# Optimization experiments

Measured on AMD Instinct MI355X. Metric: run time of the kernel, lower is better.

The kernel has to match this reference:

```python
import jax, jax.numpy as jnp
import numpy as np

EPS = 1e-5
COMMIT_W = 2.0
LATENT = 64


def _conv1d(x, w, b, stride, padding):
    # x: [B,C,T], w: [O,I,K] (torch Conv1d layout)
    y = jax.lax.conv_general_dilated(x, w, (stride,), [(padding, padding)],
                                     dimension_numbers=('NCH', 'OIH', 'NCH'))
    return y + b[None, :, None]


def _bn(x, g, b):
    # training-mode BatchNorm1d: batch statistics over (B, T) per channel
    mu = x.mean(axis=(0, 2), keepdims=True)
    var = x.var(axis=(0, 2), keepdims=True)
    return (x - mu) * jax.lax.rsqrt(var + EPS) * g[None, :, None] + b[None, :, None]


def setup_inputs():
    key = jax.random.key(0)
    ks = jax.random.split(key, 10)
    B, T, D, K = 8, 10240, LATENT, 8192
    f32 = jnp.float32
    def n(k, shape, scale):
        return jax.random.normal(k, shape, dtype=f32) * scale
    return {
        'x': jax.random.normal(ks[0], (B, 1, T), dtype=f32),
        'enc_w1': n(ks[1], (16, 1, 5), 0.3), 'enc_b1': jnp.zeros((16,), f32),
        'bn1_g': jnp.ones((16,), f32), 'bn1_b': jnp.zeros((16,), f32),
        'enc_w2': n(ks[2], (32, 16, 5), 0.1), 'enc_b2': jnp.zeros((32,), f32),
        'bn2_g': jnp.ones((32,), f32), 'bn2_b': jnp.zeros((32,), f32),
        'enc_w3': n(ks[3], (64, 32, 25), 0.05), 'enc_b3': jnp.zeros((64,), f32),
        'bn3_g': jnp.ones((64,), f32), 'bn3_b': jnp.zeros((64,), f32),
        'codebook': jax.random.normal(ks[4], (K, D), dtype=f32),
        'dec_wt': n(ks[5], (64, 64, 25), 0.05),  # torch ConvTranspose1d [in,out,k]
        'dbn1_g': jnp.ones((64,), f32), 'dbn1_b': jnp.zeros((64,), f32),
        'dec_w2': n(ks[6], (64, 64, 5), 0.08), 'dec_b2': jnp.zeros((64,), f32),
        'dbn2_g': jnp.ones((64,), f32), 'dbn2_b': jnp.zeros((64,), f32),
        'dec_w3': n(ks[7], (1, 64, 1), 0.1), 'dec_b3': jnp.zeros((1,), f32),
    }


def reference(x, enc_w1, enc_b1, bn1_g, bn1_b, enc_w2, enc_b2, bn2_g, bn2_b,
              enc_w3, enc_b3, bn3_g, bn3_b, codebook, dec_wt, dbn1_g, dbn1_b,
              dec_w2, dec_b2, dbn2_g, dbn2_b, dec_w3, dec_b3):
    # ---- encoder ----
    h = jax.nn.silu(_conv1d(x, enc_w1, enc_b1, 1, 2))
    h = _bn(h, bn1_g, bn1_b)
    h = jax.nn.silu(_conv1d(h, enc_w2, enc_b2, 1, 2))
    h = _bn(h, bn2_g, bn2_b)
    h = jnp.tanh(_conv1d(h, enc_w3, enc_b3, 5, 12))
    z = _bn(h, bn3_g, bn3_b)                       # [B, 64, L]
    B, _, L = z.shape
    # ---- VQ: euclidean nearest-neighbor against codebook ----
    zf = z.transpose(0, 2, 1).reshape(-1, LATENT)  # [N, D]
    d = ((zf * zf).sum(-1, keepdims=True)
         - 2.0 * zf @ codebook.T
         + (codebook * codebook).sum(-1)[None, :])  # [N, K]
    idx = jnp.argmin(d, axis=-1)                   # [N]
    q = codebook[idx]                              # [N, D]
    commit_loss = COMMIT_W * jnp.mean((jax.lax.stop_gradient(q) - zf) ** 2)
    q_st = zf + jax.lax.stop_gradient(q - zf)      # straight-through
    zq = q_st.reshape(B, L, LATENT).transpose(0, 2, 1)  # [B, 64, L]
    # ---- decoder ----
    # ConvTranspose1d(k=25, s=5, p=12) == dilated conv with flipped kernel
    wconv = jnp.flip(dec_wt, -1).transpose(1, 0, 2)     # [out, in, k]
    h = jax.lax.conv_general_dilated(zq, wconv, (1,), [(12, 12)], lhs_dilation=(5,),
                                     dimension_numbers=('NCH', 'OIH', 'NCH'))
    h = jax.nn.silu(h)
    h = _bn(h, dbn1_g, dbn1_b)
    h = jax.nn.silu(_conv1d(h, dec_w2, dec_b2, 1, 2))
    h = _bn(h, dbn2_g, dbn2_b)
    recon = _conv1d(h, dec_w3, dec_b3, 1, 0)       # [B, 1, ~T]
    T = x.shape[2]
    cur = recon.shape[2]
    if cur > T:
        recon = recon[:, :, :T]
    elif cur < T:
        recon = jnp.pad(recon, ((0, 0), (0, 0), (0, T - cur)))
    return recon, idx.reshape(B, L), commit_loss
```

## Files before the change

### kernel.cpp

```cpp
#include <hip/hip_runtime.h>
#include <hip/hip_bf16.h>

#define DEV __device__ __forceinline__

typedef __attribute__((ext_vector_type(8))) short s8v;
typedef __attribute__((ext_vector_type(16))) float f32x16;
typedef __attribute__((address_space(1))) const unsigned int u32g;
typedef __attribute__((address_space(3))) unsigned int u32l;

DEV void gl_lds(const void* g, void* l){
  __builtin_amdgcn_global_load_lds((u32g*)g, (u32l*)l, 16, 0, 0);
}

DEV float siluf(float x){ return x / (1.f + expf(-x)); }

DEV float wredsum(float v){
  #pragma unroll
  for(int m = 32; m; m >>= 1) v += __shfl_xor(v, m);
  return v;
}

DEV unsigned short bf16rne(float f){
  unsigned int u = __float_as_uint(f);
  u += 0x7FFFu + ((u >> 16) & 1u);
  return (unsigned short)(u >> 16);
}
DEV float bf16tof(unsigned short h){ return __uint_as_float(((unsigned int)h) << 16); }

DEV unsigned umed3(unsigned a, unsigned b, unsigned c){
  unsigned d;
  asm("v_med3_u32 %0, %1, %2, %3" : "=v"(d) : "v"(a), "v"(b), "v"(c));
  return d;
}

#define S1 0
#define Q1 16
#define S2 32
#define Q2 64
#define S3 96
#define Q3 160
#define S4 224
#define Q4 288
#define S5 352
#define Q5 416
#define SLOSS 480
#define NSTATF 512

#define EPSQ 6u
#define NCHUNK 8

__global__ void k_prep(const float* ew3, const float* dwt, float* w3t, float* dwtt,
                       unsigned short* wb7){
  const int n1 = 64*32*25, n2 = 64*64*25;
  for(int i = blockIdx.x*blockDim.x + threadIdx.x; i < n1+n2; i += gridDim.x*blockDim.x){
    if(i < n1){
      int c = i/(32*25), r = i - c*(32*25), ii = r/25, k = r - ii*25;
      w3t[(ii*25 + k)*64 + c] = ew3[i];
    } else {
      int j = i - n1;
      int ii = j/(64*25), r = j - ii*(64*25), o = r/25, k = r - o*25;
      float w = dwt[j];
      dwtt[(ii*25 + k)*64 + o] = w;
      wb7[((size_t)(k*64 + o))*64 + ii] = bf16rne(w);
    }
  }
}

__global__ void k_prep2(const float* __restrict__ cb, unsigned short* __restrict__ cbsw,
                        float* __restrict__ cnw, float* __restrict__ cnw2,
                        unsigned short* __restrict__ cbb, int* cnt){
  if(blockIdx.x == 0 && threadIdx.x == 0) *cnt = 0;
  int j = blockIdx.x*256 + threadIdx.x;
  if(j < 8192){
    float nrm = 0.f;
    unsigned swz = (j & 15) << 4;
    char* rowp = (char*)cbsw + (size_t)j*256;
    #pragma unroll
    for(int k = 0; k < 64; k++){
      float x = cb[(size_t)j*64 + k];
      unsigned short hi = bf16rne(x);
      float lo = x - bf16tof(hi);
      *(unsigned short*)(rowp + (((unsigned)(2*k)) ^ swz)) = hi;
      *(unsigned short*)(rowp + (((unsigned)(128 + 2*k)) ^ swz)) = bf16rne(lo);
      cbb[(size_t)j*64 + k] = hi;
      nrm = fmaf(x, x, nrm);
    }
    cnw[j] = nrm;
    cnw2[j] = (nrm + 1024.f) * 256.f;
  }
}

__global__ void k1(const float* __restrict__ x, const float* __restrict__ w1,
                   const float* __restrict__ b1, float* __restrict__ h1, float* stats){
  __shared__ float xs[136];
  __shared__ float ssum[16], ssq[16];
  int tid = threadIdx.x, b = blockIdx.y, t0 = blockIdx.x*128;
  if(tid < 16){ ssum[tid] = 0.f; ssq[tid] = 0.f; }
  for(int i = tid; i < 132; i += 256){
    int t = t0 + i - 2;
    xs[i] = (t >= 0 && t < 10240) ? x[b*10240 + t] : 0.f;
  }
  __syncthreads();
  int c = tid & 15, sgrp = tid >> 4;
  float w[5];
  #pragma unroll
  for(int k = 0; k < 5; k++) w[k] = w1[c*5 + k];
  float bias = b1[c];
  float outv[8];
  float ps = 0.f, pq = 0.f;
  #pragma unroll
  for(int s = 0; s < 8; s++){
    float a = bias;
    #pragma unroll
    for(int k = 0; k < 5; k++) a = fmaf(w[k], xs[sgrp*8 + s + k], a);
    a = siluf(a);
    outv[s] = a;
    ps += a; pq += a*a;
  }
  float* op = h1 + ((size_t)(b*16 + c))*10240 + t0 + sgrp*8;
  #pragma unroll
  for(int q = 0; q < 2; q++)
    *(float4*)(op + q*4) = make_float4(outv[q*4], outv[q*4+1], outv[q*4+2], outv[q*4+3]);
  ps += __shfl_xor(ps, 16); pq += __shfl_xor(pq, 16);
  ps += __shfl_xor(ps, 32); pq += __shfl_xor(pq, 32);
  if((tid & 48) == 0){ atomicAdd(&ssum[c], ps); atomicAdd(&ssq[c], pq); }
  __syncthreads();
  if(tid < 16){ atomicAdd(stats+S1+tid, ssum[tid]); atomicAdd(stats+Q1+tid, ssq[tid]); }
}

__global__ __launch_bounds__(256) void k2(const float* __restrict__ h1,
                   const float* __restrict__ w2, const float* __restrict__ b2,
                   const float* __restrict__ g1, const float* __restrict__ bb1,
                   float* __restrict__ h2out, float* stats){
  __shared__ float hs[16][136];
  __shared__ float A1s[16], B1s[16];
  __shared__ float ssum[32], ssq[32];
  int tid = threadIdx.x, b = blockIdx.y, t0 = blockIdx.x*128;
  if(tid < 16){
    float mu = stats[S1+tid]/81920.f;
    float var = stats[Q1+tid]/81920.f - mu*mu;
    float rs = rsqrtf(var + 1e-5f);
    A1s[tid] = rs*g1[tid];
    B1s[tid] = bb1[tid] - mu*rs*g1[tid];
  }
  if(tid < 32){ ssum[tid] = 0.f; ssq[tid] = 0.f; }
  __syncthreads();
  {
    int ch = tid >> 4, j0 = tid & 15;
    float A = A1s[ch], B = B1s[ch];
    const float* hp = h1 + ((size_t)(b*16 + ch))*10240;
    for(int j = j0; j < 132; j += 16){
      int t = t0 + j - 2;
      hs[ch][j] = (t >= 0 && t < 10240) ? hp[t]*A + B : 0.f;
    }
  }
  __syncthreads();
  int c = tid & 31, tgrp = tid >> 5;
  int tb = tgrp*16;
  float acc[16];
  float bias = b2[c];
  #pragma unroll
  for(int s = 0; s < 16; s++) acc[s] = bias;
  for(int ic = 0; ic < 4; ic++){
    float wf[20];
    const float* wp = w2 + c*80 + ic*20;
    #pragma unroll
    for(int q = 0; q < 5; q++) *(float4*)(wf + q*4) = *(const float4*)(wp + q*4);
    #pragma unroll
    for(int di = 0; di < 4; di++){
      int i = ic*4 + di;
      float z[20];
      #pragma unroll
      for(int q = 0; q < 5; q++) *(float4*)(z + q*4) = *(const float4*)(&hs[i][tb] + q*4);
      float w0 = wf[di*5], w1 = wf[di*5+1], w2v = wf[di*5+2], w3 = wf[di*5+3], w4 = wf[di*5+4];
      #pragma unroll
      for(int s = 0; s < 16; s++)
        acc[s] = fmaf(w0, z[s], fmaf(w1, z[s+1], fmaf(w2v, z[s+2],
                 fmaf(w3, z[s+3], fmaf(w4, z[s+4], acc[s])))));
    }
  }
  float ps = 0.f, pq = 0.f;
  #pragma unroll
  for(int s = 0; s < 16; s++){
    float a = siluf(acc[s]);
    acc[s] = a;
    ps += a; pq += a*a;
  }
  float* op = h2out + ((size_t)(b*32 + c))*10240 + t0 + tb;
  #pragma unroll
  for(int q = 0; q < 4; q++)
    *(float4*)(op + q*4) = make_float4(acc[q*4], acc[q*4+1], acc[q*4+2], acc[q*4+3]);
  ps += __shfl_xor(ps, 32); pq += __shfl_xor(pq, 32);
  if((tid & 32) == 0){ atomicAdd(&ssum[c], ps); atomicAdd(&ssq[c], pq); }
  __syncthreads();
  if(tid < 32){ atomicAdd(stats+S2+tid, ssum[tid]); atomicAdd(stats+Q2+tid, ssq[tid]); }
}

__global__ void k3(const float* __restrict__ h2, const float* __restrict__ w3t,
                   const float* __restrict__ eb3, const float* __restrict__ g2,
                   const float* __restrict__ bb2, float* __restrict__ zn, float* stats){
  __shared__ __align__(16) float X[5*32*24];
  __shared__ float A2[32], B2[32];
  __shared__ float ssum[64], ssq[64];
  int tid = threadIdx.x, b = blockIdx.y, l0 = blockIdx.x*16;
  if(tid < 32){
    float mu = stats[S2+tid]/81920.f;
    float var = stats[Q2+tid]/81920.f - mu*mu;
    float rs = rsqrtf(var + 1e-5f);
    A2[tid] = rs*g2[tid];
    B2[tid] = bb2[tid] - mu*rs*g2[tid];
  }
  if(tid < 64){ ssum[tid] = 0.f; ssq[tid] = 0.f; }
  __syncthreads();
  for(int i2 = tid; i2 < 5*32*20; i2 += 256){
    int kk = i2/640;
    int r  = i2 - kk*640;
    int ch = r/20, m = r - ch*20;
    int t = 5*(l0 + m) + kk - 12;
    float v = 0.f;
    if(t >= 0 && t < 10240) v = h2[((b*32+ch)*10240)+t]*A2[ch] + B2[ch];
    X[(kk*32+ch)*24 + m] = v;
  }
  __syncthreads();
  int c = tid & 63, lslot = tid >> 6;
  float acc[4];
  float bias = eb3[c];
  #pragma unroll
  for(int s = 0; s < 4; s++) acc[s] = bias;
  for(int i = 0; i < 32; i++){
    #pragma unroll
    for(int kk = 0; kk < 5; kk++){
      const float* xp = &X[(kk*32+i)*24 + lslot*4];
      float4 za = *(const float4*)(xp);
      float4 zb = *(const float4*)(xp + 4);
      float z[8] = {za.x,za.y,za.z,za.w,zb.x,zb.y,zb.z,zb.w};
      #pragma unroll
      for(int kap = 0; kap < 5; kap++){
        float w = w3t[(i*25 + kap*5 + kk)*64 + c];
        #pragma unroll
        for(int s = 0; s < 4; s++) acc[s] = fmaf(w, z[s+kap], acc[s]);
      }
    }
  }
  float ls = 0.f, lq = 0.f;
  #pragma unroll
  for(int s = 0; s < 4; s++){
    int l = l0 + lslot*4 + s;
    float a = tanhf(acc[s]);
    zn[((b*2048 + l)*64) + c] = a;
    ls += a; lq += a*a;
  }
  atomicAdd(&ssum[c], ls); atomicAdd(&ssq[c], lq);
  __syncthreads();
  if(tid < 64){ atomicAdd(stats+S3+tid, ssum[tid]); atomicAdd(stats+Q3+tid, ssq[tid]); }
}

__global__ __launch_bounds__(256, 3) void k5m(const float* __restrict__ zn,
    const unsigned short* __restrict__ cbsw, const float* __restrict__ cnw2,
    const float* __restrict__ g3, const float* __restrict__ b3,
    const float* __restrict__ stats,
    unsigned int* __restrict__ pbk, unsigned int* __restrict__ psk){
  __shared__ __align__(16) unsigned char cbuf[2][16384];
  __shared__ float A3s[64], B3s[64];
  int tid = threadIdx.x;
  int chunk = blockIdx.x;
  int m0 = blockIdx.y * 128;
  int lane = tid & 63, wr = tid >> 6;
  int h = lane >> 5, cll = lane & 31;
  int row = m0 + wr*32 + cll;

  if(tid < 64){
    float mu = stats[S3+tid]/16384.f;
    float var = stats[Q3+tid]/16384.f - mu*mu;
    float rs = rsqrtf(var + 1e-5f);
    A3s[tid] = rs*g3[tid];
    B3s[tid] = b3[tid] - mu*rs*g3[tid];
  }

  int c0 = chunk * 1024;
  const char* csrc = (const char*)cbsw + (size_t)c0*256;
  #pragma unroll
  for(int c2 = 0; c2 < 4; c2++)
    gl_lds(csrc + c2*4096 + tid*16, &cbuf[0][0] + c2*4096 + tid*16);
  __syncthreads();

  s8v ah[4], al[4];
  const float* zp = zn + (size_t)row*64;
  #pragma unroll
  for(int s = 0; s < 4; s++){
    int koff = s*16 + h*8;
    float4 v0 = *(const float4*)(zp + koff);
    float4 v1 = *(const float4*)(zp + koff + 4);
    float vv[8] = {v0.x,v0.y,v0.z,v0.w,v1.x,v1.y,v1.z,v1.w};
    #pragma unroll
    for(int i = 0; i < 8; i++){
      float v = fmaf(vv[i], A3s[koff + i], B3s[koff + i]);
      unsigned short hi = bf16rne(v);
      ah[s][i] = (short)hi;
      al[s][i] = (short)bf16rne(v - bf16tof(hi));
    }
  }

  unsigned int bk[16], sk[16];
  #pragma unroll
  for(int r = 0; r < 16; r++){ bk[r] = 0xFFFFFFFFu; sk[r] = 0xFFFFFFFFu; }
  f32x16 zv;
  #pragma unroll
  for(int i = 0; i < 16; i++) zv[i] = 0.f;

  unsigned swz = (unsigned)(cll & 15) << 4;
  for(int tile = 0; tile < 16; ++tile){
    int bsel = tile & 1;
    if(tile < 15){
      const char* ns = csrc + (size_t)(tile+1)*16384;
      #pragma unroll
      for(int c2 = 0; c2 < 4; c2++)
        gl_lds(ns + c2*4096 + tid*16, &cbuf[bsel^1][0] + c2*4096 + tid*16);
    }
    #pragma unroll
    for(int half = 0; half < 2; half++){
      const unsigned char* bp = &cbuf[bsel][0] + (half*32 + cll)*256;
      s8v bh[4], bl[4];
      #pragma unroll
      for(int s = 0; s < 4; s++){
        bh[s] = *(const s8v*)(bp + (((unsigned)(s*32 + h*16)) ^ swz));
        bl[s] = *(const s8v*)(bp + (((unsigned)(128 + s*32 + h*16)) ^ swz));
      }
      unsigned col = (unsigned)(c0 + tile*64 + half*32 + cll);
      float cnv2 = cnw2[col];
      f32x16 a1 = __builtin_amdgcn_mfma_f32_32x32x16_bf16(ah[0], bh[0], zv, 0, 0, 0);
      f32x16 a2 = __builtin_amdgcn_mfma_f32_32x32x16_bf16(al[0], bh[0], zv, 0, 0, 0);
      a2 = __builtin_amdgcn_mfma_f32_32x32x16_bf16(ah[0], bl[0], a2, 0, 0, 0);
      #pragma unroll
      for(int s = 1; s < 4; s++){
        a1 = __builtin_amdgcn_mfma_f32_32x32x16_bf16(ah[s], bh[s], a1, 0, 0, 0);
        a2 = __builtin_amdgcn_mfma_f32_32x32x16_bf16(al[s], bh[s], a2, 0, 0, 0);
        a2 = __builtin_amdgcn_mfma_f32_32x32x16_bf16(ah[s], bl[s], a2, 0, 0, 0);
      }
      #pragma unroll
      for(int r = 0; r < 16; r++){
        float q = fmaf(-512.f, a1[r], cnv2);
        q = fmaf(-512.f, a2[r], q);
        q = fminf(q, 524287.f);
        unsigned k = (((unsigned)q) << 13) | col;
        unsigned nb = bk[r] < k ? bk[r] : k;
        sk[r] = umed3(sk[r], bk[r], k);
        bk[r] = nb;
      }
    }
    __syncthreads();
  }

  #pragma unroll
  for(int m = 1; m <= 16; m <<= 1){
    #pragma unroll
    for(int r = 0; r < 16; r++){
      unsigned int ob = (unsigned int)__shfl_xor((int)bk[r], m);
      unsigned int os = (unsigned int)__shfl_xor((int)sk[r], m);
      unsigned int s2 = sk[r] < os ? sk[r] : os;
      sk[r] = umed3(s2, bk[r], ob);
      bk[r] = bk[r] < ob ? bk[r] : ob;
    }
  }
  if(cll == 0){
    size_t base = (size_t)chunk*16384 + m0 + wr*32 + 4*h;
    #pragma unroll
    for(int r = 0; r < 16; r++){
      int lr = (r&3) + 8*(r>>2);
      pbk[base + lr] = bk[r];
      psk[base + lr] = sk[r];
    }
  }
}

__global__ void k5r(const unsigned int* __restrict__ pbk,
                    const unsigned int* __restrict__ psk, int* __restrict__ idxw,
                    float* __restrict__ out_idx, int* __restrict__ list, int* cnt){
  int row = blockIdx.x*256 + threadIdx.x;
  unsigned int bk = pbk[row], sk = psk[row];
  #pragma unroll
  for(int c = 1; c < NCHUNK; c++){
    unsigned int ob = pbk[(size_t)c*16384 + row];
    unsigned int os = psk[(size_t)c*16384 + row];
    unsigned int s2 = sk < os ? sk : os;
    sk = umed3(s2, bk, ob);
    bk = bk < ob ? bk : ob;
  }
  int idx = (int)(bk & 0x1FFFu);
  idxw[row] = idx;
  out_idx[row] = (float)idx;
  if((sk >> 13) - (bk >> 13) <= EPSQ){
    int p = atomicAdd(cnt, 1);
    list[p] = row;
  }
}

__global__ __launch_bounds__(256) void k5x(const float* __restrict__ zn,
    const float* __restrict__ cb, const float* __restrict__ cnw,
    const float* __restrict__ g3, const float* __restrict__ b3,
    const float* __restrict__ stats,
    const int* __restrict__ list, const int* cnt,
    float* __restrict__ pxd, int* __restrict__ pxi){
  __shared__ float A3s[64], B3s[64];
  int tid = threadIdx.x;
  if(tid < 64){
    float mu = stats[S3+tid]/16384.f;
    float var = stats[Q3+tid]/16384.f - mu*mu;
    float rs = rsqrtf(var + 1e-5f);
    A3s[tid] = rs*g3[tid];
    B3s[tid] = b3[tid] - mu*rs*g3[tid];
  }
  __syncthreads();
  int chunk = blockIdx.x;
  int n = *cnt;
  int rgrp = tid >> 6, cs = tid & 63;
  int c0 = chunk * 1024;
  for(int bat = blockIdx.y; bat*4 < n; bat += 256){
    int e = bat*4 + rgrp;
    int ec = e < n ? e : n-1;
    int row = list[ec];
    float4 zr[16];
    const float4* zp = (const float4*)(zn + (size_t)row*64);
    #pragma unroll
    for(int q = 0; q < 16; q++){
      float4 v = zp[q];
      v.x = fmaf(v.x, A3s[q*4+0], B3s[q*4+0]);
      v.y = fmaf(v.y, A3s[q*4+1], B3s[q*4+1]);
      v.z = fmaf(v.z, A3s[q*4+2], B3s[q*4+2]);
      v.w = fmaf(v.w, A3s[q*4+3], B3s[q*4+3]);
      zr[q] = v;
    }
    float bd = 3.4e38f; int bi = 0;
    for(int step = 0; step < 16; step++){
      int j = c0 + step*64 + cs;
      const float4* cp = (const float4*)(cb + (size_t)j*64);
      float cnv = cnw[j];
      float da = 0.f, db = 0.f;
      #pragma unroll
      for(int q = 0; q < 16; q += 2){
        float4 ca = cp[q], cb4 = cp[q+1];
        da = fmaf(ca.x, zr[q].x, da);  da = fmaf(ca.y, zr[q].y, da);
        da = fmaf(ca.z, zr[q].z, da);  da = fmaf(ca.w, zr[q].w, da);
        db = fmaf(cb4.x, zr[q+1].x, db); db = fmaf(cb4.y, zr[q+1].y, db);
        db = fmaf(cb4.z, zr[q+1].z, db); db = fmaf(cb4.w, zr[q+1].w, db);
      }
      float d = fmaf(-2.f, da + db, cnv);
      if(d < bd){ bd = d; bi = j; }
    }
    #pragma unroll
    for(int m = 1; m <= 32; m <<= 1){
      float od = __shfl_xor(bd, m);
      int   oi = __shfl_xor(bi, m);
      if(od < bd || (od == bd && oi < bi)){ bd = od; bi = oi; }
    }
    if(cs == 0 && e < n){
      pxd[(size_t)chunk*16384 + e] = bd;
      pxi[(size_t)chunk*16384 + e] = bi;
    }
  }
}

__global__ void k5x2(const float* __restrict__ pxd, const int* __restrict__ pxi,
                     const int* __restrict__ list, const int* cnt,
                     int* __restrict__ idxw, float* __restrict__ out_idx){
  int e = blockIdx.x*256 + threadIdx.x;
  int n = *cnt;
  if(e >= n) return;
  float bd = pxd[e]; int bi = pxi[e];
  #pragma unroll
  for(int c = 1; c < NCHUNK; c++){
    float od = pxd[(size_t)c*16384 + e];
    int   oi = pxi[(size_t)c*16384 + e];
    if(od < bd || (od == bd && oi < bi)){ bd = od; bi = oi; }
  }
  int row = list[e];
  idxw[row] = bi;
  out_idx[row] = (float)bi;
}

__global__ void k_loss(const float* __restrict__ zn, const float* __restrict__ cb,
                       const float* __restrict__ g3, const float* __restrict__ b3,
                       const int* __restrict__ idxw, float* stats){
  __shared__ float A3s[64], B3s[64];
  int tid = threadIdx.x;
  if(tid < 64){
    float mu = stats[S3+tid]/16384.f;
    float var = stats[Q3+tid]/16384.f - mu*mu;
    float rs = rsqrtf(var + 1e-5f);
    A3s[tid] = rs*g3[tid];
    B3s[tid] = b3[tid] - mu*rs*g3[tid];
  }
  __syncthreads();
  int row = blockIdx.x*256 + tid;
  int code = idxw[row];
  const float* cp = cb + (size_t)code*64;
  const float* zp = zn + (size_t)row*64;
  float s = 0.f;
  #pragma unroll
  for(int k = 0; k < 64; k++){
    float v = fmaf(zp[k], A3s[k], B3s[k]);
    float dd = cp[k] - v;
    s = fmaf(dd, dd, s);
  }
  float tot = wredsum(s);
  if((tid & 63) == 0) atomicAdd(stats + SLOSS, tot);
}

__global__ __launch_bounds__(320) void k7m(const int* __restrict__ idxp,
    const unsigned short* __restrict__ cbb, const unsigned short* __restrict__ wb7,
    unsigned short* __restrict__ h4t, float* stats){
  __shared__ __align__(16) unsigned char lA[37*128];
  __shared__ float tb[5*64*33];
  __shared__ float ssum[64], ssq[64];
  int tid = threadIdx.x, b = blockIdx.y, u0 = blockIdx.x*32;
  if(tid < 64){ ssum[tid] = 0.f; ssq[tid] = 0.f; }
  {
    int m = tid >> 3, part = tid & 7;
    if(m < 37){
      int u = u0 - 2 + m;
      uint4 val = make_uint4(0,0,0,0);
      if(u >= 0 && u < 2048){
        int code = idxp[b*2048 + u];
        val = *(const uint4*)((const char*)cbb + (size_t)code*128 + part*16);
      }
      *(uint4*)(lA + m*128 + (((unsigned)(part*16)) ^ (((unsigned)m & 7) << 4))) = val;
    }
  }
  __syncthreads();
  int lane = tid & 63, h = lane >> 5, cl = lane & 31;
  int v = tid >> 6;
  const int km[5]  = {2,3,4,0,1};
  const int ovv[5] = {2,2,2,3,3};
  f32x16 acc0, acc1;
  #pragma unroll
  for(int i = 0; i < 16; i++){ acc0[i] = 0.f; acc1[i] = 0.f; }
  #pragma unroll
  for(int r = 0; r < 5; r++){
    int off = ovv[v] - r + 2;
    int m = cl + off;
    unsigned aswz = ((unsigned)m & 7) << 4;
    int k = km[v] + 5*r;
    const char* b0p = (const char*)wb7 + (size_t)(k*64 + cl)*128;
    const char* b1p = b0p + 32*128;
    #pragma unroll
    for(int s = 0; s < 4; s++){
      unsigned o = (unsigned)(s*32 + h*16);
      s8v a  = *(const s8v*)(lA + m*128 + (o ^ aswz));
      s8v b0 = *(const s8v*)(b0p + o);
      s8v b1 = *(const s8v*)(b1p + o);
      acc0 = __builtin_amdgcn_mfma_f32_32x32x16_bf16(a, b0, acc0, 0, 0, 0);
      acc1 = __builtin_amdgcn_mfma_f32_32x32x16_bf16(a, b1, acc1, 0, 0, 0);
    }
  }
  float ps0 = 0.f, pq0 = 0.f, ps1 = 0.f, pq1 = 0.f;
  #pragma unroll
  for(int r = 0; r < 16; r++){
    int ul = (r&3) + 8*(r>>2) + 4*h;
    int u = u0 + ul;
    float v0 = siluf(acc0[r]), v1 = siluf(acc1[r]);
    tb[(v*64 + cl)*33 + ul]      = v0;
    tb[(v*64 + 32 + cl)*33 + ul] = v1;
    if(v == 0 || u < 2047){ ps0 += v0; pq0 += v0*v0; ps1 += v1; pq1 += v1*v1; }
  }
  atomicAdd(&ssum[cl], ps0);      atomicAdd(&ssq[cl], pq0);
  atomicAdd(&ssum[32 + cl], ps1); atomicAdd(&ssq[32 + cl], pq1);
  __syncthreads();
  if(tid < 64){ atomicAdd(stats+S4+tid, ssum[tid]); atomicAdd(stats+Q4+tid, ssq[tid]); }
  #pragma unroll
  for(int j = 0; j < 16; j++){
    int flat = j*320 + tid;
    int tl = flat >> 5;
    int chp = flat & 31;
    int t = u0*5 + tl;
    if(t < 10236){
      int vv = tl % 5, ul = tl / 5;
      float f0 = tb[(vv*64 + 2*chp)*33 + ul];
      float f1 = tb[(vv*64 + 2*chp + 1)*33 + ul];
      unsigned int pk = (unsigned int)bf16rne(f0) | ((unsigned int)bf16rne(f1) << 16);
      size_t rowb = ((size_t)b*10248 + 2 + t)*128;
      *(unsigned int*)((char*)h4t + rowb + (((unsigned)(4*chp)) ^ (((unsigned)t & 7) << 4))) = pk;
    }
  }
}

__global__ void k8w(const float* __restrict__ w2d, const float* __restrict__ b2d,
                    const float* __restrict__ g4, const float* __restrict__ bb4,
                    const float* __restrict__ stats, unsigned short* __restrict__ wbt,
                    float* __restrict__ beta, unsigned int* __restrict__ h4tz){
  __shared__ float A4[64], B4[64];
  int tid = threadIdx.x;
  for(int i = tid; i < 3072; i += 256){
    int b = i / 384, r = i - b*384;
    int row12 = r >> 5, word = r & 31;
    int row = row12 < 2 ? row12 : 10236 + row12;
    h4tz[((size_t)b*10248 + row)*32 + word] = 0u;
  }
  if(tid < 64){
    float mu = stats[S4+tid]/81888.f;
    float var = stats[Q4+tid]/81888.f - mu*mu;
    float rs = rsqrtf(var + 1e-5f);
    A4[tid] = rs*g4[tid];
    B4[tid] = bb4[tid] - mu*rs*g4[tid];
  }
  __syncthreads();
  for(int e = tid; e < 64*64*5; e += 256){
    int c = e/320, r = e - c*320, i = r/5, k = r - i*5;
    unsigned short hw = bf16rne(w2d[e] * A4[i]);
    int row = k*64 + c;
    *(unsigned short*)((char*)wbt + (size_t)row*128 + (((unsigned)(2*i)) ^ (((unsigned)c & 7) << 4))) = hw;
  }
  if(tid < 64){
    float s = b2d[tid];
    for(int i = 0; i < 64; i++){
      float wsum = 0.f;
      #pragma unroll
      for(int k = 0; k < 5; k++) wsum += w2d[(tid*64 + i)*5 + k];
      s += wsum * B4[i];
    }
    beta[tid] = s;
  }
}

__global__ __launch_bounds__(256) void k8(const unsigned short* __restrict__ h4t,
    const unsigned short* __restrict__ wbt, const float* __restrict__ beta,
    unsigned short* __restrict__ h5b, float* stats){
  __shared__ __align__(16) unsigned char lA[68*128];
  __shared__ float ssum[64], ssq[64];
  int tid = threadIdx.x, b = blockIdx.y, t0 = blockIdx.x*64;
  if(tid < 64){ ssum[tid] = 0.f; ssq[tid] = 0.f; }
  const char* srcA = (const char*)h4t + ((size_t)b*10248 + t0)*128;
  #pragma unroll
  for(int c2 = 0; c2 < 2; c2++)
    gl_lds(srcA + c2*4096 + tid*16, lA + c2*4096 + tid*16);
  if(tid < 32) gl_lds(srcA + 8192 + tid*16, lA + 8192 + tid*16);
  __syncthreads();

  int lane = tid & 63, h = lane >> 5, cl = lane & 31;
  int widx = tid >> 6;
  int wt0 = (widx >> 1) * 32;
  int wch = (widx & 1) * 32;
  f32x16 acc;
  #pragma unroll
  for(int i = 0; i < 16; i++) acc[i] = 0.f;
  unsigned bswz = (unsigned)(cl & 7) << 4;
  #pragma unroll
  for(int k = 0; k < 5; k++){
    int l = wt0 + cl + k;
    unsigned aswz = (unsigned)((l + 6) & 7) << 4;
    const char* bp = (const char*)wbt + (size_t)(k*64 + wch + cl)*128;
    #pragma unroll
    for(int s = 0; s < 4; s++){
      unsigned o = (unsigned)(s*32 + h*16);
      s8v a  = *(const s8v*)(lA + l*128 + (o ^ aswz));
      s8v bb = *(const s8v*)(bp + (o ^ bswz));
      acc = __builtin_amdgcn_mfma_f32_32x32x16_bf16(a, bb, acc, 0, 0, 0);
    }
  }
  float bet = beta[wch + cl];
  float ps = 0.f, pq = 0.f;
  #pragma unroll
  for(int r = 0; r < 16; r++){
    int t = t0 + wt0 + (r&3) + 8*(r>>2) + 4*h;
    float v0 = siluf(acc[r] + bet);
    if(t < 10236){
      h5b[((size_t)b*10240 + t)*64 + wch + cl] = bf16rne(v0);
      ps += v0; pq += v0*v0;
    }
  }
  atomicAdd(&ssum[wch + cl], ps); atomicAdd(&ssq[wch + cl], pq);
  __syncthreads();
  if(tid < 64){ atomicAdd(stats+S5+tid, ssum[tid]); atomicAdd(stats+Q5+tid, ssq[tid]); }
}

__global__ void k9(const unsigned short* __restrict__ h5b, const float* __restrict__ w3,
                   const float* __restrict__ b3, const float* __restrict__ g5,
                   const float* __restrict__ bb5, const float* stats,
                   float* __restrict__ out){
  __shared__ float WA[64], WB[64];
  int tid = threadIdx.x;
  if(blockIdx.x == 0 && blockIdx.y == 0 && tid == 0)
    out[98304] = 2.f * stats[SLOSS] / 1048576.f;
  if(tid < 64){
    float mu = stats[S5+tid]/81888.f;
    float var = stats[Q5+tid]/81888.f - mu*mu;
    float rs = rsqrtf(var + 1e-5f);
    float A = rs*g5[tid], B = bb5[tid] - mu*rs*g5[tid];
    float w = w3[tid];
    WA[tid] = w*A; WB[tid] = w*B;
  }
  __syncthreads();
  int b = blockIdx.y;
  int t = blockIdx.x*256 + tid;
  float acc = b3[0];
  if(t < 10236){
    const unsigned short* hp = h5b + ((size_t)b*10240 + t)*64;
    #pragma unroll
    for(int q = 0; q < 8; q++){
      uint4 u = *(const uint4*)(hp + q*8);
      unsigned int ua[4] = {u.x, u.y, u.z, u.w};
      #pragma unroll
      for(int w = 0; w < 4; w++){
        int c = q*8 + w*2;
        acc += WA[c]*bf16tof((unsigned short)(ua[w] & 0xFFFFu)) + WB[c];
        acc += WA[c+1]*bf16tof((unsigned short)(ua[w] >> 16)) + WB[c+1];
      }
    }
  } else acc = 0.f;
  out[b*10240 + t] = acc;
}

extern "C" void kernel_launch(void* const* d_in, const int* in_sizes, int n_in,
                              void* d_out, int out_size, void* d_ws, size_t ws_size,
                              hipStream_t stream){
  const float* x   = (const float*)d_in[0];
  const float* ew1 = (const float*)d_in[1];
  const float* eb1 = (const float*)d_in[2];
  const float* g1  = (const float*)d_in[3];
  const float* bb1 = (const float*)d_in[4];
  const float* ew2 = (const float*)d_in[5];
  const float* eb2 = (const float*)d_in[6];
  const float* g2  = (const float*)d_in[7];
  const float* bb2 = (const float*)d_in[8];
  const float* ew3 = (const float*)d_in[9];
  const float* eb3 = (const float*)d_in[10];
  const float* g3  = (const float*)d_in[11];
  const float* bb3 = (const float*)d_in[12];
  const float* cb  = (const float*)d_in[13];
  const float* dwt = (const float*)d_in[14];
  const float* g4  = (const float*)d_in[15];
  const float* bb4 = (const float*)d_in[16];
  const float* w2d = (const float*)d_in[17];
  const float* b2d = (const float*)d_in[18];
  const float* g5  = (const float*)d_in[19];
  const float* bb5 = (const float*)d_in[20];
  const float* w3d = (const float*)d_in[21];
  const float* b3d = (const float*)d_in[22];

  char* ws = (char*)d_ws;
  float* h1   = (float*)(ws + 0);
  unsigned short* cbsw = (unsigned short*)(ws + 0);
  float* cnw  = (float*)(ws + 2097152);
  float* cnw2 = (float*)(ws + 2129920);
  float* h2   = (float*)(ws + 5242880);
  float* zn   = (float*)(ws + 15728640);
  unsigned short* h4t = (unsigned short*)(ws + 0);
  unsigned short* h5b = (unsigned short*)(ws + 20971520);
  int*   list = (int*)  (ws + 20971520);
  int*   cnt  = (int*)  (ws + 21037056);
  unsigned int* pbk = (unsigned int*)(ws + 21037312);
  unsigned int* psk = (unsigned int*)(ws + 21561600);
  float* pxd  = (float*)(ws + 22085888);
  int*   pxi  = (int*)  (ws + 22610176);
  unsigned short* wbt = (unsigned short*)(ws + 31457280);
  float* beta = (float*)(ws + 31498240);
  unsigned short* wb7 = (unsigned short*)(ws + 32000000);
  unsigned short* cbb = (unsigned short*)(ws + 32300032);
  float* w3t  = (float*)(ws + 41934848);
  float* dwtt = (float*)(ws + 42139648);
  int*   idxw = (int*)  (ws + 42549248);
  float* stats= (float*)(ws + 42614784);
  if(ws_size < 42616832) return;

  float* out = (float*)d_out;

  hipMemsetAsync(stats, 0, NSTATF*4, stream);
  k_prep<<<600, 256, 0, stream>>>(ew3, dwt, w3t, dwtt, wb7);
  k1<<<dim3(80,8), 256, 0, stream>>>(x, ew1, eb1, h1, stats);
  k2<<<dim3(80,8), 256, 0, stream>>>(h1, ew2, eb2, g1, bb1, h2, stats);
  k_prep2<<<32, 256, 0, stream>>>(cb, cbsw, cnw, cnw2, cbb, cnt);
  k3<<<dim3(128,8), 256, 0, stream>>>(h2, w3t, eb3, g2, bb2, zn, stats);
  k5m<<<dim3(NCHUNK,128), 256, 0, stream>>>(zn, cbsw, cnw2, g3, bb3, stats, pbk, psk);
  k5r<<<64, 256, 0, stream>>>(pbk, psk, idxw, out + 81920, list, cnt);
  k5x<<<dim3(NCHUNK,256), 256, 0, stream>>>(zn, cb, cnw, g3, bb3, stats, list, cnt, pxd, pxi);
  k5x2<<<64, 256, 0, stream>>>(pxd, pxi, list, cnt, idxw, out + 81920);
  k_loss<<<64, 256, 0, stream>>>(zn, cb, g3, bb3, idxw, stats);
  k7m<<<dim3(64,8), 320, 0, stream>>>(idxw, cbb, wb7, h4t, stats);
  k8w<<<1, 256, 0, stream>>>(w2d, b2d, g4, bb4, stats, wbt, beta, (unsigned int*)h4t);
  k8<<<dim3(160,8), 256, 0, stream>>>(h4t, wbt, beta, h5b, stats);
  k9<<<dim3(40,8), 256, 0, stream>>>(h5b, w3d, b3d, g5, bb5, stats, out);
}
```

Measured before the change: 330.3 us.

## Widen k3 output tile, vectorize weight loads, merge k5m MFMA accumulators

The k3 encoder conv now computes 8 outputs per thread over 32-position blocks and reads its five tap weights per (channel, phase) as one packed vector from a re-laid-out weight array. This gives more reuse of each weight and LDS value and fewer scalar global loads, at the cost of more registers and a grid of half the size. In k5m the two accumulator chains are merged into one, freeing 16 VGPRs, and launch bounds are raised to 4 blocks per CU for occupancy. The merged chain is a longer serial MFMA dependency, and the hi/lo partial sums are now added in a different order. The unused dwtt transpose is also dropped.

Result: slower. 337.4 us (+2.2%).

```diff
diff --git a/kernel.cpp b/kernel.cpp
--- a/kernel.cpp
+++ b/kernel.cpp
@@ -49,19 +49,18 @@
 #define EPSQ 6u
 #define NCHUNK 8
 
-__global__ void k_prep(const float* ew3, const float* dwt, float* w3t, float* dwtt,
+__global__ void k_prep(const float* ew3, const float* dwt, float* w3t8,
                        unsigned short* wb7){
   const int n1 = 64*32*25, n2 = 64*64*25;
   for(int i = blockIdx.x*blockDim.x + threadIdx.x; i < n1+n2; i += gridDim.x*blockDim.x){
     if(i < n1){
       int c = i/(32*25), r = i - c*(32*25), ii = r/25, k = r - ii*25;
-      w3t[(ii*25 + k)*64 + c] = ew3[i];
+      int kk = k % 5, kap = k / 5;
+      w3t8[(((size_t)(ii*5 + kk))*64 + c)*8 + kap] = ew3[i];
     } else {
       int j = i - n1;
       int ii = j/(64*25), r = j - ii*(64*25), o = r/25, k = r - o*25;
-      float w = dwt[j];
-      dwtt[(ii*25 + k)*64 + o] = w;
-      wb7[((size_t)(k*64 + o))*64 + ii] = bf16rne(w);
+      wb7[((size_t)(k*64 + o))*64 + ii] = bf16rne(dwt[j]);
     }
   }
 }
@@ -196,13 +195,13 @@
   if(tid < 32){ atomicAdd(stats+S2+tid, ssum[tid]); atomicAdd(stats+Q2+tid, ssq[tid]); }
 }
 
-__global__ void k3(const float* __restrict__ h2, const float* __restrict__ w3t,
+__global__ void k3(const float* __restrict__ h2, const float* __restrict__ w3t8,
                    const float* __restrict__ eb3, const float* __restrict__ g2,
                    const float* __restrict__ bb2, float* __restrict__ zn, float* stats){
-  __shared__ __align__(16) float X[5*32*24];
+  __shared__ __align__(16) float X[5*32*40];
   __shared__ float A2[32], B2[32];
   __shared__ float ssum[64], ssq[64];
-  int tid = threadIdx.x, b = blockIdx.y, l0 = blockIdx.x*16;
+  int tid = threadIdx.x, b = blockIdx.y, l0 = blockIdx.x*32;
   if(tid < 32){
     float mu = stats[S2+tid]/81920.f;
     float var = stats[Q2+tid]/81920.f - mu*mu;
@@ -212,40 +211,44 @@
   }
   if(tid < 64){ ssum[tid] = 0.f; ssq[tid] = 0.f; }
   __syncthreads();
-  for(int i2 = tid; i2 < 5*32*20; i2 += 256){
-    int kk = i2/640;
-    int r  = i2 - kk*640;
-    int ch = r/20, m = r - ch*20;
+  for(int i2 = tid; i2 < 5*32*36; i2 += 256){
+    int kk = i2/1152;
+    int r  = i2 - kk*1152;
+    int ch = r/36, m = r - ch*36;
     int t = 5*(l0 + m) + kk - 12;
     float v = 0.f;
     if(t >= 0 && t < 10240) v = h2[((b*32+ch)*10240)+t]*A2[ch] + B2[ch];
-    X[(kk*32+ch)*24 + m] = v;
+    X[(kk*32+ch)*40 + m] = v;
   }
   __syncthreads();
   int c = tid & 63, lslot = tid >> 6;
-  float acc[4];
+  float acc[8];
   float bias = eb3[c];
   #pragma unroll
-  for(int s = 0; s < 4; s++) acc[s] = bias;
+  for(int s = 0; s < 8; s++) acc[s] = bias;
   for(int i = 0; i < 32; i++){
     #pragma unroll
     for(int kk = 0; kk < 5; kk++){
-      const float* xp = &X[(kk*32+i)*24 + lslot*4];
-      float4 za = *(const float4*)(xp);
-      float4 zb = *(const float4*)(xp + 4);
-      float z[8] = {za.x,za.y,za.z,za.w,zb.x,zb.y,zb.z,zb.w};
+      const float* xp = &X[(kk*32+i)*40 + lslot*8];
+      float z[12];
+      #pragma unroll
+      for(int q = 0; q < 3; q++) *(float4*)(z + q*4) = *(const float4*)(xp + q*4);
+      const float* wp = w3t8 + (((size_t)(i*5 + kk))*64 + c)*8;
+      float wv[5];
+      *(float4*)wv = *(const float4*)wp;
+      wv[4] = wp[4];
       #pragma unroll
       for(int kap = 0; kap < 5; kap++){
-        float w = w3t[(i*25 + kap*5 + kk)*64 + c];
+        float w = wv[kap];
         #pragma unroll
-        for(int s = 0; s < 4; s++) acc[s] = fmaf(w, z[s+kap], acc[s]);
+        for(int s = 0; s < 8; s++) acc[s] = fmaf(w, z[s+kap], acc[s]);
       }
     }
   }
   float ls = 0.f, lq = 0.f;
   #pragma unroll
-  for(int s = 0; s < 4; s++){
-    int l = l0 + lslot*4 + s;
+  for(int s = 0; s < 8; s++){
+    int l = l0 + lslot*8 + s;
     float a = tanhf(acc[s]);
     zn[((b*2048 + l)*64) + c] = a;
     ls += a; lq += a*a;
@@ -255,7 +258,7 @@
   if(tid < 64){ atomicAdd(stats+S3+tid, ssum[tid]); atomicAdd(stats+Q3+tid, ssq[tid]); }
 }
 
-__global__ __launch_bounds__(256, 3) void k5m(const float* __restrict__ zn,
+__global__ __launch_bounds__(256, 4) void k5m(const float* __restrict__ zn,
     const unsigned short* __restrict__ cbsw, const float* __restrict__ cnw2,
     const float* __restrict__ g3, const float* __restrict__ b3,
     const float* __restrict__ stats,
@@ -328,19 +331,18 @@
       }
       unsigned col = (unsigned)(c0 + tile*64 + half*32 + cll);
       float cnv2 = cnw2[col];
-      f32x16 a1 = __builtin_amdgcn_mfma_f32_32x32x16_bf16(ah[0], bh[0], zv, 0, 0, 0);
-      f32x16 a2 = __builtin_amdgcn_mfma_f32_32x32x16_bf16(al[0], bh[0], zv, 0, 0, 0);
-      a2 = __builtin_amdgcn_mfma_f32_32x32x16_bf16(ah[0], bl[0], a2, 0, 0, 0);
+      f32x16 a = __builtin_amdgcn_mfma_f32_32x32x16_bf16(ah[0], bl[0], zv, 0, 0, 0);
+      a = __builtin_amdgcn_mfma_f32_32x32x16_bf16(al[0], bh[0], a, 0, 0, 0);
+      a = __builtin_amdgcn_mfma_f32_32x32x16_bf16(ah[0], bh[0], a, 0, 0, 0);
       #pragma unroll
       for(int s = 1; s < 4; s++){
-        a1 = __builtin_amdgcn_mfma_f32_32x32x16_bf16(ah[s], bh[s], a1, 0, 0, 0);
-        a2 = __builtin_amdgcn_mfma_f32_32x32x16_bf16(al[s], bh[s], a2, 0, 0, 0);
-        a2 = __builtin_amdgcn_mfma_f32_32x32x16_bf16(ah[s], bl[s], a2, 0, 0, 0);
+        a = __builtin_amdgcn_mfma_f32_32x32x16_bf16(ah[s], bl[s], a, 0, 0, 0);
+        a = __builtin_amdgcn_mfma_f32_32x32x16_bf16(al[s], bh[s], a, 0, 0, 0);
+        a = __builtin_amdgcn_mfma_f32_32x32x16_bf16(ah[s], bh[s], a, 0, 0, 0);
       }
       #pragma unroll
       for(int r = 0; r < 16; r++){
-        float q = fmaf(-512.f, a1[r], cnv2);
-        q = fmaf(-512.f, a2[r], q);
+        float q = fmaf(-512.f, a[r], cnv2);
         q = fminf(q, 524287.f);
         unsigned k = (((unsigned)q) << 13) | col;
         unsigned nb = bk[r] < k ? bk[r] : k;
@@ -755,8 +757,7 @@
   float* beta = (float*)(ws + 31498240);
   unsigned short* wb7 = (unsigned short*)(ws + 32000000);
   unsigned short* cbb = (unsigned short*)(ws + 32300032);
-  float* w3t  = (float*)(ws + 41934848);
-  float* dwtt = (float*)(ws + 42139648);
+  float* w3t8 = (float*)(ws + 41934848);
   int*   idxw = (int*)  (ws + 42549248);
   float* stats= (float*)(ws + 42614784);
   if(ws_size < 42616832) return;
@@ -764,11 +765,11 @@
   float* out = (float*)d_out;
 
   hipMemsetAsync(stats, 0, NSTATF*4, stream);
-  k_prep<<<600, 256, 0, stream>>>(ew3, dwt, w3t, dwtt, wb7);
+  k_prep<<<600, 256, 0, stream>>>(ew3, dwt, w3t8, wb7);
   k1<<<dim3(80,8), 256, 0, stream>>>(x, ew1, eb1, h1, stats);
   k2<<<dim3(80,8), 256, 0, stream>>>(h1, ew2, eb2, g1, bb1, h2, stats);
   k_prep2<<<32, 256, 0, stream>>>(cb, cbsw, cnw, cnw2, cbb, cnt);
-  k3<<<dim3(128,8), 256, 0, stream>>>(h2, w3t, eb3, g2, bb2, zn, stats);
+  k3<<<dim3(64,8), 256, 0, stream>>>(h2, w3t8, eb3, g2, bb2, zn, stats);
   k5m<<<dim3(NCHUNK,128), 256, 0, stream>>>(zn, cbsw, cnw2, g3, bb3, stats, pbk, psk);
   k5r<<<64, 256, 0, stream>>>(pbk, psk, idxw, out + 81920, list, cnt);
   k5x<<<dim3(NCHUNK,256), 256, 0, stream>>>(zn, cb, cnw, g3, bb3, stats, list, cnt, pxd, pxi);
```
